# Kernel tuning notes

Measured on AMD Instinct MI355X. Metric: run time of the kernel, lower is better.

## Reference

```python
import jax, jax.numpy as jnp
import numpy as np
from jax import lax

B, L, D = 2, 512, 1024
N, K, R = 16, 4, 64
DEPTH, V, MLP = 4, 50000, 4096
HALF = D // 2


def _ln(x, s, b, eps=1e-5):
    m = x.mean(-1, keepdims=True)
    v = ((x - m) ** 2).mean(-1, keepdims=True)
    return (x - m) / jnp.sqrt(v + eps) * s + b


def _selective_scan(x, wx, wz, wp, cw, dtw, dtb, a_log, dpar, wout):
    bsz, seqlen, d = x.shape
    x_res = x @ wx.T
    z = x @ wz.T
    p = x @ wp.T  # [B,L,R+2N]
    dt_u, b_proj, c_proj = p[..., :R], p[..., R:R + N], p[..., R + N:]
    dt = jax.nn.softplus(dt_u @ dtw.T + dtb)  # [B,L,D]
    # causal depthwise conv (torch pads K-1 both sides then slices :L == left-pad K-1)
    conv = lax.conv_general_dilated(x_res.transpose(0, 2, 1), cw[:, None, :],
                                    (1,), [(K - 1, 0)], feature_group_count=d)
    u = jax.nn.silu(conv.transpose(0, 2, 1))  # [B,L,D]
    a = -jnp.exp(a_log)  # [D,N]
    a_t = jnp.exp(dt[..., None] * a)  # [B,L,D,N] (ZOH discretize)
    b_t = jnp.where(jnp.abs(a) < 1e-8, dt[..., None], (a_t - 1.0) / (a + 1e-10))
    inp = b_t * b_proj[:, :, None, :] * u[..., None]  # [B,L,D,N]

    def step(h, xs):
        at, it, ct = xs
        h = at * h + it
        return h, jnp.einsum('bn,bdn->bd', ct, h)

    h0 = jnp.zeros((bsz, d, N), a_t.dtype)
    _, ys = lax.scan(step, h0, (a_t.transpose(1, 0, 2, 3),
                                inp.transpose(1, 0, 2, 3),
                                c_proj.transpose(1, 0, 2)))
    y = ys.transpose(1, 0, 2)  # [B,L,D]
    y = (y + u * dpar) * jax.nn.silu(z)
    return y @ wout.T


def _forward(input_ids, timesteps, emb_table, tw1, tb1, tw2, tb2,
             ln1_s, ln1_b, wx, wz, wp, conv_w, dt_w, dt_b, A_log, Dp, wout,
             ln2_s, ln2_b, mlp_w1, mlp_b1, mlp_w2, mlp_b2,
             lnout_s, lnout_b, head_w, head_b):
    # sinusoidal time embedding [B,D]
    freq = jnp.exp(jnp.arange(HALF, dtype=jnp.float32) * (-np.log(10000.0) / (HALF - 1)))
    e = timesteps.astype(jnp.float32)[:, None] * freq
    temb = jnp.concatenate([jnp.sin(e), jnp.cos(e)], axis=-1)
    temb = jax.nn.silu(temb @ tw1.T + tb1) @ tw2.T + tb2
    x = emb_table[input_ids] + temb[:, None, :]
    for i in range(DEPTH):
        h = _selective_scan(_ln(x, ln1_s[i], ln1_b[i]), wx[i], wz[i], wp[i],
                            conv_w[i], dt_w[i], dt_b[i], A_log[i], Dp[i], wout[i])
        x = x + h
        m = _ln(x, ln2_s[i], ln2_b[i])
        m = jax.nn.gelu(m @ mlp_w1[i].T + mlp_b1[i], approximate=False) @ mlp_w2[i].T + mlp_b2[i]
        x = x + m
    x = _ln(x, lnout_s, lnout_b)
    return x @ head_w.T + head_b  # [B,L,V]


def setup_inputs() -> dict:
    key = jax.random.key(0)
    ks = jax.random.split(key, 20)

    def nrm(k, shape, scale=0.02):
        return jax.random.normal(k, shape, jnp.float32) * scale

    dt_std = R ** (-0.5)
    inp = {
        'input_ids': jax.random.randint(ks[0], (B, L), 0, V + 1),
        'timesteps': jax.random.randint(ks[1], (B,), 0, 100),
        'emb_table': nrm(ks[2], (V + 1, D)),
        'tw1': nrm(ks[3], (4 * D, D)), 'tb1': jnp.zeros((4 * D,), jnp.float32),
        'tw2': nrm(ks[4], (D, 4 * D)), 'tb2': jnp.zeros((D,), jnp.float32),
        'ln1_s': jnp.ones((DEPTH, D), jnp.float32), 'ln1_b': jnp.zeros((DEPTH, D), jnp.float32),
        'wx': nrm(ks[5], (DEPTH, D, D)),
        'wz': nrm(ks[6], (DEPTH, D, D)),
        'wp': nrm(ks[7], (DEPTH, R + 2 * N, D)),
        'conv_w': nrm(ks[8], (DEPTH, D, K), 0.1),
        'dt_w': jax.random.uniform(ks[9], (DEPTH, D, R), jnp.float32, -dt_std, dt_std),
        'dt_b': jnp.full((DEPTH, D), float(np.log(np.expm1(0.01))), jnp.float32),
        'A_log': jnp.tile(jnp.log(jnp.arange(1, N + 1, dtype=jnp.float32))[None, None, :], (DEPTH, D, 1)),
        'Dp': jnp.ones((DEPTH, D), jnp.float32),
        'wout': nrm(ks[10], (DEPTH, D, D)),
        'ln2_s': jnp.ones((DEPTH, D), jnp.float32), 'ln2_b': jnp.zeros((DEPTH, D), jnp.float32),
        'mlp_w1': nrm(ks[11], (DEPTH, MLP, D)), 'mlp_b1': jnp.zeros((DEPTH, MLP), jnp.float32),
        'mlp_w2': nrm(ks[12], (DEPTH, D, MLP)), 'mlp_b2': jnp.zeros((DEPTH, D), jnp.float32),
        'lnout_s': jnp.ones((D,), jnp.float32), 'lnout_b': jnp.zeros((D,), jnp.float32),
        'head_w': nrm(ks[13], (V, D)), 'head_b': jnp.zeros((V,), jnp.float32),
    }
    return inp


def reference(input_ids, timesteps, emb_table, tw1, tb1, tw2, tb2,
              ln1_s, ln1_b, wx, wz, wp, conv_w, dt_w, dt_b, A_log, Dp, wout,
              ln2_s, ln2_b, mlp_w1, mlp_b1, mlp_w2, mlp_b2,
              lnout_s, lnout_b, head_w, head_b):
    return _forward(input_ids, timesteps, emb_table, tw1, tb1, tw2, tb2,
                    ln1_s, ln1_b, wx, wz, wp, conv_w, dt_w, dt_b, A_log, Dp, wout,
                    ln2_s, ln2_b, mlp_w1, mlp_b1, mlp_w2, mlp_b2,
                    lnout_s, lnout_b, head_w, head_b)
```

## Files before the change

kernel.cpp:

```cpp
#include <hip/hip_runtime.h>

typedef unsigned short u16;
typedef __attribute__((ext_vector_type(8))) __bf16 bf16x8;
typedef __attribute__((ext_vector_type(4))) float floatx4;

#define B_ 2
#define L_ 512
#define D_ 1024
#define N_ 16
#define R_ 64
#define DEPTH_ 4
#define V_ 50000
#define MLP_ 4096
#define MROWS (B_ * L_)
#define SCAN_C 32
#define SCAN_S (L_ / SCAN_C)

#define SWZ(b) ((b) ^ ((((b) >> 7) & 7) << 4))

__device__ __forceinline__ float b2f(u16 u) {
    unsigned int i = ((unsigned int)u) << 16;
    return __builtin_bit_cast(float, i);
}
__device__ __forceinline__ u16 f2b(float f) {
    return __builtin_bit_cast(u16, (__bf16)f);
}
__device__ __forceinline__ uint2 f4_to_b4(float4 v) {
    u16 a = f2b(v.x), b = f2b(v.y), c = f2b(v.z), d = f2b(v.w);
    uint2 r;
    r.x = (unsigned int)a | ((unsigned int)b << 16);
    r.y = (unsigned int)c | ((unsigned int)d << 16);
    return r;
}
__device__ __forceinline__ void async16(const void* g, void* l) {
    __builtin_amdgcn_global_load_lds(
        (const __attribute__((address_space(1))) void*)g,
        (__attribute__((address_space(3))) void*)l, 16, 0, 0);
}
template <int Ncnt>
__device__ __forceinline__ void waitcnt_vm() {
    if constexpr (Ncnt == 0) asm volatile("s_waitcnt vmcnt(0)" ::: "memory");
    else if constexpr (Ncnt == 2) asm volatile("s_waitcnt vmcnt(2)" ::: "memory");
    else if constexpr (Ncnt == 3) asm volatile("s_waitcnt vmcnt(3)" ::: "memory");
    else if constexpr (Ncnt == 4) asm volatile("s_waitcnt vmcnt(4)" ::: "memory");
    else if constexpr (Ncnt == 6) asm volatile("s_waitcnt vmcnt(6)" ::: "memory");
    else if constexpr (Ncnt == 8) asm volatile("s_waitcnt vmcnt(8)" ::: "memory");
    else asm volatile("s_waitcnt vmcnt(0)" ::: "memory");
}
__device__ __forceinline__ float silu_f(float v) { return v / (1.f + expf(-v)); }
__device__ __forceinline__ float gelu_f(float v) {
    return 0.5f * v * (1.f + erff(v * 0.7071067811865476f));
}
__device__ __forceinline__ float softplus_f(float v) {
    return fmaxf(v, 0.f) + log1pf(expf(-fabsf(v)));
}

__global__ __launch_bounds__(256) void cvt_kernel(const float* __restrict__ in,
                                                  u16* __restrict__ out, const int n8) {
    const int i = blockIdx.x * 256 + threadIdx.x;
    if (i >= n8) return;
    const float4 a = *reinterpret_cast<const float4*>(&in[(size_t)i * 8]);
    const float4 b = *reinterpret_cast<const float4*>(&in[(size_t)i * 8 + 4]);
    uint4 o;
    uint2 lo = f4_to_b4(a), hi = f4_to_b4(b);
    o.x = lo.x; o.y = lo.y; o.z = hi.x; o.w = hi.y;
    *reinterpret_cast<uint4*>(&out[(size_t)i * 8]) = o;
}

template <int BM, int BN, int ACT, int RES, int PIPEOK, typename AT, typename WT, typename OUT>
__global__ __launch_bounds__(256) void gemm_bt(
    const AT* __restrict__ A, const int lda,
    const WT* __restrict__ W, const WT* __restrict__ W2,
    const float* __restrict__ bias,
    OUT* __restrict__ out, OUT* __restrict__ out2,
    const int N, const int K, const int nt, const int gsz) {
    constexpr int BK = 64;
    constexpr int MI = BM / 32;
    constexpr int NI = BN / 32;
    constexpr int WM = BM / 2;
    constexpr bool PIPE = PIPEOK && (sizeof(AT) == 2) && (sizeof(WT) == 2);
    __shared__ alignas(16) u16 lA[(PIPE ? 2 : 1) * BM * BK];
    __shared__ alignas(16) u16 lW[(PIPE ? 2 : 1) * BN * BK];
    const int tid = threadIdx.x;
    const int lane = tid & 63, wv = tid >> 6;
    const int bid = blockIdx.x;

    int mI, nI;
    if (gsz > 0) {
        const int mtt = gridDim.x / nt;
        const int fullG = nt / gsz;
        const int fullBlocks = fullG * gsz * mtt;
        if (bid < fullBlocks) {
            const int per = gsz * mtt;
            const int g = bid / per, r = bid % per;
            mI = r / gsz;
            nI = g * gsz + r % gsz;
        } else {
            const int rem = nt - fullG * gsz;
            const int r = bid - fullBlocks;
            mI = r / rem;
            nI = fullG * gsz + r % rem;
        }
    } else {
        mI = bid / nt;
        nI = bid % nt;
    }
    const int m0 = mI * BM;
    int n0 = nI * BN;
    const WT* Wp = W;
    OUT* op = out;
    if (W2 != nullptr && n0 >= N) {
        Wp = W2;
        op = out2;
        n0 -= N;
    }
    const int wr = wv >> 1, wc = wv & 1;
    const int lr = lane & 15, kg = lane >> 4;

    floatx4 acc[MI][NI];
#pragma unroll
    for (int i = 0; i < MI; ++i)
#pragma unroll
        for (int j = 0; j < NI; ++j) {
            floatx4 z4 = {0.f, 0.f, 0.f, 0.f};
            acc[i][j] = z4;
        }

    const int T = K / BK;

    if constexpr (PIPE) {
        constexpr int NEWER = BM / 32 + BN / 32;
        auto issue = [&](int t) {
            const int buf = t & 1;
            const int kt = t * BK;
#pragma unroll
            for (int c = wv; c < BM / 8; c += 4) {
                const int dst = c * 1024 + lane * 16;
                const int lg = SWZ(dst);
                const int row = lg >> 7, colb = lg & 127;
                async16((const char*)A + ((size_t)(m0 + row) * lda + kt) * 2 + colb,
                        (char*)lA + buf * BM * 128 + c * 1024);
            }
#pragma unroll
            for (int c = wv; c < BN / 8; c += 4) {
                const int dst = c * 1024 + lane * 16;
                const int lg = SWZ(dst);
                const int row = lg >> 7, colb = lg & 127;
                int rn = n0 + row;
                rn = (rn < N) ? rn : (N - 1);
                async16((const char*)Wp + ((size_t)rn * K + kt) * 2 + colb,
                        (char*)lW + buf * BN * 128 + c * 1024);
            }
        };
        issue(0);
        for (int t = 0; t < T; ++t) {
            if (t + 1 < T) {
                issue(t + 1);
                waitcnt_vm<NEWER>();
            } else {
                waitcnt_vm<0>();
            }
            __builtin_amdgcn_s_barrier();
            __builtin_amdgcn_sched_barrier(0);
            const char* bA = (const char*)lA + (t & 1) * BM * 128;
            const char* bW = (const char*)lW + (t & 1) * BN * 128;
#pragma unroll
            for (int kk = 0; kk < 2; ++kk) {
                bf16x8 aF[MI], bF[NI];
#pragma unroll
                for (int mi = 0; mi < MI; ++mi)
                    aF[mi] = *reinterpret_cast<const bf16x8*>(
                        bA + SWZ((wr * WM + mi * 16 + lr) * 128 + kk * 64 + kg * 16));
#pragma unroll
                for (int ni = 0; ni < NI; ++ni)
                    bF[ni] = *reinterpret_cast<const bf16x8*>(
                        bW + SWZ((wc * (BN / 2) + ni * 16 + lr) * 128 + kk * 64 + kg * 16));
#pragma unroll
                for (int mi = 0; mi < MI; ++mi)
#pragma unroll
                    for (int ni = 0; ni < NI; ++ni)
                        acc[mi][ni] = __builtin_amdgcn_mfma_f32_16x16x32_bf16(
                            aF[mi], bF[ni], acc[mi][ni], 0, 0, 0);
            }
            __builtin_amdgcn_sched_barrier(0);
            if (t + 1 < T) __builtin_amdgcn_s_barrier();
        }
    } else {
        for (int t = 0; t < T; ++t) {
            const int kt = t * BK;
            if (t) __syncthreads();
            if constexpr (sizeof(AT) == 2) {
#pragma unroll
                for (int c = wv; c < BM / 8; c += 4) {
                    const int dst = c * 1024 + lane * 16;
                    const int lg = SWZ(dst);
                    const int row = lg >> 7, colb = lg & 127;
                    async16((const char*)A + ((size_t)(m0 + row) * lda + kt) * 2 + colb,
                            (char*)lA + c * 1024);
                }
            } else {
                constexpr int ACHF = (BM * BK) / 1024;
                float4 raF[ACHF];
#pragma unroll
                for (int i = 0; i < ACHF; ++i) {
                    const int idx = tid + i * 256;
                    const int row = idx >> 4, c4 = (idx & 15) * 4;
                    raF[i] = *reinterpret_cast<const float4*>(&A[(size_t)(m0 + row) * lda + kt + c4]);
                }
#pragma unroll
                for (int i = 0; i < ACHF; ++i) {
                    const int idx = tid + i * 256;
                    const int row = idx >> 4, c4 = (idx & 15) * 4;
                    *reinterpret_cast<uint2*>((char*)lA + SWZ(row * 128 + c4 * 2)) = f4_to_b4(raF[i]);
                }
            }
            if constexpr (sizeof(WT) == 2) {
#pragma unroll
                for (int c = wv; c < BN / 8; c += 4) {
                    const int dst = c * 1024 + lane * 16;
                    const int lg = SWZ(dst);
                    const int row = lg >> 7, colb = lg & 127;
                    int rn = n0 + row;
                    rn = (rn < N) ? rn : (N - 1);
                    async16((const char*)Wp + ((size_t)rn * K + kt) * 2 + colb,
                            (char*)lW + c * 1024);
                }
            } else {
                constexpr int WCHF = (BN * BK) / 1024;
                float4 rwF[WCHF];
#pragma unroll
                for (int i = 0; i < WCHF; ++i) {
                    const int idx = tid + i * 256;
                    const int row = idx >> 4, c4 = (idx & 15) * 4;
                    int rn = n0 + row;
                    rn = (rn < N) ? rn : (N - 1);
                    rwF[i] = *reinterpret_cast<const float4*>(&Wp[(size_t)rn * K + kt + c4]);
                }
#pragma unroll
                for (int i = 0; i < WCHF; ++i) {
                    const int idx = tid + i * 256;
                    const int row = idx >> 4, c4 = (idx & 15) * 4;
                    *reinterpret_cast<uint2*>((char*)lW + SWZ(row * 128 + c4 * 2)) = f4_to_b4(rwF[i]);
                }
            }
            __syncthreads();
#pragma unroll
            for (int kk = 0; kk < 2; ++kk) {
                bf16x8 aF[MI], bF[NI];
#pragma unroll
                for (int mi = 0; mi < MI; ++mi)
                    aF[mi] = *reinterpret_cast<const bf16x8*>(
                        (const char*)lA + SWZ((wr * WM + mi * 16 + lr) * 128 + kk * 64 + kg * 16));
#pragma unroll
                for (int ni = 0; ni < NI; ++ni)
                    bF[ni] = *reinterpret_cast<const bf16x8*>(
                        (const char*)lW + SWZ((wc * (BN / 2) + ni * 16 + lr) * 128 + kk * 64 + kg * 16));
#pragma unroll
                for (int mi = 0; mi < MI; ++mi)
#pragma unroll
                    for (int ni = 0; ni < NI; ++ni)
                        acc[mi][ni] = __builtin_amdgcn_mfma_f32_16x16x32_bf16(
                            aF[mi], bF[ni], acc[mi][ni], 0, 0, 0);
            }
        }
    }

#pragma unroll
    for (int mi = 0; mi < MI; ++mi) {
        const int rb = m0 + wr * WM + mi * 16 + kg * 4;
#pragma unroll
        for (int r = 0; r < 4; ++r) {
            const size_t rowoff = (size_t)(rb + r) * (size_t)N;
#pragma unroll
            for (int ni = 0; ni < NI; ++ni) {
                const int col = n0 + wc * (BN / 2) + ni * 16 + lr;
                if (col >= N) continue;
                float v = acc[mi][ni][r] + (bias ? bias[col] : 0.f);
                if constexpr (ACT == 1) v = gelu_f(v);
                if constexpr (ACT == 2) v = softplus_f(v);
                const size_t o = rowoff + (size_t)col;
                if constexpr (RES) {
                    op[o] += v;
                } else if constexpr (sizeof(OUT) == 2) {
                    op[o] = f2b(v);
                } else {
                    op[o] = v;
                }
            }
        }
    }
}

__global__ __launch_bounds__(256) void temb0_kernel(const int* __restrict__ ts,
                                                    float* __restrict__ temb0) {
    int i = blockIdx.x * 256 + threadIdx.x;
    if (i >= B_ * D_) return;
    int b = i >> 10, k = i & 1023;
    float t = (float)ts[b];
    int h = (k < 512) ? k : (k - 512);
    float f = expf((float)h * (-9.210340371976184f / 511.f));
    float e = t * f;
    temb0[i] = (k < 512) ? sinf(e) : cosf(e);
}

template <int ACTV>
__global__ __launch_bounds__(256) void rowdot_kernel(const float* __restrict__ in,
                                                     const float* __restrict__ W,
                                                     const float* __restrict__ bias,
                                                     float* __restrict__ out,
                                                     const int Ncols, const int K) {
    const int g = (blockIdx.x * 256 + threadIdx.x) >> 6;
    const int lane = threadIdx.x & 63;
    if (g >= B_ * Ncols) return;
    const int b = g / Ncols, j = g % Ncols;
    const float* xr = in + (size_t)b * K;
    const float* wr = W + (size_t)j * K;
    float s = 0.f;
    for (int k = lane; k < K; k += 64) s += xr[k] * wr[k];
#pragma unroll
    for (int o = 32; o; o >>= 1) s += __shfl_xor(s, o);
    if (lane == 0) {
        float v = s + bias[j];
        if (ACTV == 1) v = silu_f(v);
        out[(size_t)b * Ncols + j] = v;
    }
}

__global__ __launch_bounds__(256) void embed_kernel(const int* __restrict__ ids,
                                                    const float* __restrict__ emb,
                                                    const float* __restrict__ temb2,
                                                    float* __restrict__ x) {
    const int gid = blockIdx.x * 256 + threadIdx.x;
    const int d8 = gid & 127;
    const int row = gid >> 7;
    const int b = row >> 9;
    const int d0 = d8 * 8;
    const int id = ids[row];
    const float4 e0 = *reinterpret_cast<const float4*>(&emb[(size_t)id * D_ + d0]);
    const float4 e1 = *reinterpret_cast<const float4*>(&emb[(size_t)id * D_ + d0 + 4]);
    const float4 t0 = *reinterpret_cast<const float4*>(&temb2[b * D_ + d0]);
    const float4 t1 = *reinterpret_cast<const float4*>(&temb2[b * D_ + d0 + 4]);
    float4 o0, o1;
    o0.x = e0.x + t0.x; o0.y = e0.y + t0.y; o0.z = e0.z + t0.z; o0.w = e0.w + t0.w;
    o1.x = e1.x + t1.x; o1.y = e1.y + t1.y; o1.z = e1.z + t1.z; o1.w = e1.w + t1.w;
    *reinterpret_cast<float4*>(&x[(size_t)row * D_ + d0]) = o0;
    *reinterpret_cast<float4*>(&x[(size_t)row * D_ + d0 + 4]) = o1;
}

__global__ __launch_bounds__(256) void ln_kernel(const float* __restrict__ x,
                                                 const float* __restrict__ s,
                                                 const float* __restrict__ bb,
                                                 u16* __restrict__ out) {
    __shared__ float red[4];
    const int row = blockIdx.x, tid = threadIdx.x;
    const float4 v = *reinterpret_cast<const float4*>(x + (size_t)row * D_ + tid * 4);
    float sm = v.x + v.y + v.z + v.w;
#pragma unroll
    for (int o = 1; o < 64; o <<= 1) sm += __shfl_xor(sm, o);
    if ((tid & 63) == 0) red[tid >> 6] = sm;
    __syncthreads();
    const float mean = (red[0] + red[1] + red[2] + red[3]) * (1.f / 1024.f);
    __syncthreads();
    const float dx = v.x - mean, dy = v.y - mean, dz = v.z - mean, dw = v.w - mean;
    float sq = dx * dx + dy * dy + dz * dz + dw * dw;
#pragma unroll
    for (int o = 1; o < 64; o <<= 1) sq += __shfl_xor(sq, o);
    if ((tid & 63) == 0) red[tid >> 6] = sq;
    __syncthreads();
    const float var = (red[0] + red[1] + red[2] + red[3]) * (1.f / 1024.f);
    const float rs = rsqrtf(var + 1e-5f);
    const int c = tid * 4;
    const float4 sv = *reinterpret_cast<const float4*>(&s[c]);
    const float4 bv = *reinterpret_cast<const float4*>(&bb[c]);
    float4 o;
    o.x = dx * rs * sv.x + bv.x;
    o.y = dy * rs * sv.y + bv.y;
    o.z = dz * rs * sv.z + bv.z;
    o.w = dw * rs * sv.w + bv.w;
    *reinterpret_cast<uint2*>(&out[(size_t)row * D_ + c]) = f4_to_b4(o);
}

__global__ __launch_bounds__(256) void scan_p1(const u16* __restrict__ dt,
                                               const float* __restrict__ p,
                                               const u16* __restrict__ xr,
                                               const float* __restrict__ cw,
                                               const float* __restrict__ alog,
                                               float* __restrict__ Aprod,
                                               float* __restrict__ Hloc) {
    const int tid = threadIdx.x;
    const int ng = tid & 3;
    const int dl = tid >> 2;
    int blk = blockIdx.x;
    const int chunk = blk % SCAN_C; blk /= SCAN_C;
    const int dg = blk % (D_ / 64);
    const int b = blk / (D_ / 64);
    const int d = dg * 64 + dl;

    float a_v[4], inv_a[4];
#pragma unroll
    for (int j = 0; j < 4; ++j) {
        float av = -expf(alog[d * N_ + ng * 4 + j]);
        a_v[j] = av;
        inv_a[j] = 1.f / (av + 1e-10f);
    }
    const float4 cw4 = *reinterpret_cast<const float4*>(&cw[d * 4]);

    __shared__ float pbuf[SCAN_S * 32];
    const int t0 = chunk * SCAN_S;
    if (tid < SCAN_S * 8) {
        const int s = tid >> 3, off = (tid & 7) * 4;
        *reinterpret_cast<float4*>(&pbuf[s * 32 + off]) =
            *reinterpret_cast<const float4*>(&p[((size_t)(b * L_ + t0 + s)) * 96 + 64 + off]);
    }
    __syncthreads();

    const size_t base = (size_t)b * L_ * D_ + d;
    float xm3 = (t0 >= 3) ? b2f(xr[base + (size_t)(t0 - 3) * D_]) : 0.f;
    float xm2 = (t0 >= 2) ? b2f(xr[base + (size_t)(t0 - 2) * D_]) : 0.f;
    float xm1 = (t0 >= 1) ? b2f(xr[base + (size_t)(t0 - 1) * D_]) : 0.f;

    float A[4] = {1.f, 1.f, 1.f, 1.f};
    float h[4] = {0.f, 0.f, 0.f, 0.f};
#pragma unroll
    for (int s = 0; s < SCAN_S; ++s) {
        const size_t idx = base + (size_t)(t0 + s) * D_;
        const float xc = b2f(xr[idx]);
        const float uv = silu_f(cw4.x * xm3 + cw4.y * xm2 + cw4.z * xm1 + cw4.w * xc);
        xm3 = xm2; xm2 = xm1; xm1 = xc;
        const float dtv = b2f(dt[idx]);
#pragma unroll
        for (int j = 0; j < 4; ++j) {
            const float ex = fminf(dtv * a_v[j], 0.f);
            const float at = expf(ex);
            const float bt = (fabsf(a_v[j]) < 1e-8f) ? dtv : (at - 1.f) * inv_a[j];
            const float bp = pbuf[s * 32 + ng * 4 + j];
            A[j] *= at;
            h[j] = at * h[j] + bt * bp * uv;
        }
    }
    const size_t o = ((size_t)(b * SCAN_C + chunk) * D_ + d) * N_ + ng * 4;
    float4 a4 = {A[0], A[1], A[2], A[3]};
    float4 h4 = {h[0], h[1], h[2], h[3]};
    *reinterpret_cast<float4*>(&Aprod[o]) = a4;
    *reinterpret_cast<float4*>(&Hloc[o]) = h4;
}

__global__ __launch_bounds__(256) void scan_p2(const float* __restrict__ Aprod,
                                               const float* __restrict__ Hloc,
                                               float* __restrict__ Hstart) {
    const int gid = blockIdx.x * 256 + threadIdx.x;
    if (gid >= B_ * D_ * N_) return;
    const int b = gid / (D_ * N_);
    const int rem = gid % (D_ * N_);
    float H = 0.f;
#pragma unroll 8
    for (int k = 0; k < SCAN_C; ++k) {
        const size_t o = (size_t)(b * SCAN_C + k) * (D_ * N_) + rem;
        Hstart[o] = H;
        H = Aprod[o] * H + Hloc[o];
    }
}

__global__ __launch_bounds__(256) void scan_p3(const u16* __restrict__ dt,
                                               const float* __restrict__ p,
                                               const u16* __restrict__ xr,
                                               const float* __restrict__ cw,
                                               const u16* __restrict__ z,
                                               const float* __restrict__ alog,
                                               const float* __restrict__ Dp,
                                               const float* __restrict__ Hstart,
                                               u16* __restrict__ yg) {
    const int tid = threadIdx.x;
    const int ng = tid & 3;
    const int dl = tid >> 2;
    int blk = blockIdx.x;
    const int chunk = blk % SCAN_C; blk /= SCAN_C;
    const int dg = blk % (D_ / 64);
    const int b = blk / (D_ / 64);
    const int d = dg * 64 + dl;

    float a_v[4], inv_a[4];
#pragma unroll
    for (int j = 0; j < 4; ++j) {
        float av = -expf(alog[d * N_ + ng * 4 + j]);
        a_v[j] = av;
        inv_a[j] = 1.f / (av + 1e-10f);
    }
    const float Dpd = Dp[d];
    const float4 cw4 = *reinterpret_cast<const float4*>(&cw[d * 4]);

    __shared__ float pbuf[SCAN_S * 32];
    const int t0 = chunk * SCAN_S;
    if (tid < SCAN_S * 8) {
        const int s = tid >> 3, off = (tid & 7) * 4;
        *reinterpret_cast<float4*>(&pbuf[s * 32 + off]) =
            *reinterpret_cast<const float4*>(&p[((size_t)(b * L_ + t0 + s)) * 96 + 64 + off]);
    }
    __syncthreads();

    const size_t base = (size_t)b * L_ * D_ + d;
    float xm3 = (t0 >= 3) ? b2f(xr[base + (size_t)(t0 - 3) * D_]) : 0.f;
    float xm2 = (t0 >= 2) ? b2f(xr[base + (size_t)(t0 - 2) * D_]) : 0.f;
    float xm1 = (t0 >= 1) ? b2f(xr[base + (size_t)(t0 - 1) * D_]) : 0.f;

    float h[4];
    {
        const size_t o = ((size_t)(b * SCAN_C + chunk) * D_ + d) * N_ + ng * 4;
        const float4 h4 = *reinterpret_cast<const float4*>(&Hstart[o]);
        h[0] = h4.x; h[1] = h4.y; h[2] = h4.z; h[3] = h4.w;
    }

#pragma unroll
    for (int s = 0; s < SCAN_S; ++s) {
        const size_t idx = base + (size_t)(t0 + s) * D_;
        const float xc = b2f(xr[idx]);
        const float uv = silu_f(cw4.x * xm3 + cw4.y * xm2 + cw4.z * xm1 + cw4.w * xc);
        xm3 = xm2; xm2 = xm1; xm1 = xc;
        const float dtv = b2f(dt[idx]);
        float yp = 0.f;
#pragma unroll
        for (int j = 0; j < 4; ++j) {
            const float ex = fminf(dtv * a_v[j], 0.f);
            const float at = expf(ex);
            const float bt = (fabsf(a_v[j]) < 1e-8f) ? dtv : (at - 1.f) * inv_a[j];
            const float bp = pbuf[s * 32 + ng * 4 + j];
            const float cp = pbuf[s * 32 + 16 + ng * 4 + j];
            h[j] = at * h[j] + bt * bp * uv;
            yp += cp * h[j];
        }
        yp += __shfl_xor(yp, 1);
        yp += __shfl_xor(yp, 2);
        if (ng == 0) {
            const float zv = b2f(z[idx]);
            yg[idx] = f2b((yp + uv * Dpd) * silu_f(zv));
        }
    }
}

extern "C" void kernel_launch(void* const* d_in, const int* in_sizes, int n_in,
                              void* d_out, int out_size, void* d_ws, size_t ws_size,
                              hipStream_t stream) {
    (void)in_sizes; (void)n_in; (void)out_size;
    const int* ids = (const int*)d_in[0];
    const int* tsteps = (const int*)d_in[1];
    const float* emb = (const float*)d_in[2];
    const float* tw1 = (const float*)d_in[3];
    const float* tb1 = (const float*)d_in[4];
    const float* tw2 = (const float*)d_in[5];
    const float* tb2 = (const float*)d_in[6];
    const float* ln1s = (const float*)d_in[7];
    const float* ln1b = (const float*)d_in[8];
    const float* wx = (const float*)d_in[9];
    const float* wz = (const float*)d_in[10];
    const float* wp = (const float*)d_in[11];
    const float* convw = (const float*)d_in[12];
    const float* dtw = (const float*)d_in[13];
    const float* dtb = (const float*)d_in[14];
    const float* alog = (const float*)d_in[15];
    const float* dp = (const float*)d_in[16];
    const float* wo = (const float*)d_in[17];
    const float* ln2s = (const float*)d_in[18];
    const float* ln2b = (const float*)d_in[19];
    const float* mw1 = (const float*)d_in[20];
    const float* mb1 = (const float*)d_in[21];
    const float* mw2 = (const float*)d_in[22];
    const float* mb2 = (const float*)d_in[23];
    const float* lnos = (const float*)d_in[24];
    const float* lnob = (const float*)d_in[25];
    const float* hw = (const float*)d_in[26];
    const float* hb = (const float*)d_in[27];
    float* outp = (float*)d_out;

    char* w = (char*)d_ws;
    size_t used = 0;
    auto alloc = [&](size_t bytes) {
        char* pp = w;
        size_t rb = (bytes + 255) & ~(size_t)255;
        w += rb;
        used += rb;
        return pp;
    };
    float* x = (float*)alloc((size_t)MROWS * D_ * 4);
    float* t0f = (float*)alloc((size_t)B_ * D_ * 4);
    float* t1f = (float*)alloc((size_t)B_ * MLP_ * 4);
    float* t2f = (float*)alloc((size_t)B_ * D_ * 4);
    u16* xnb = (u16*)alloc((size_t)MROWS * D_ * 2);
    u16* xres = (u16*)alloc((size_t)MROWS * D_ * 2);
    u16* zb = (u16*)alloc((size_t)MROWS * D_ * 2);
    float* pf = (float*)alloc((size_t)MROWS * 96 * 4);
    u16* dtb16 = (u16*)alloc((size_t)MROWS * D_ * 2);
    u16* ygb = (u16*)alloc((size_t)MROWS * D_ * 2);
    const bool cvt_head = (ws_size >= used + (size_t)V_ * D_ * 2 + 4096);
    u16* hwb = cvt_head ? (u16*)alloc((size_t)V_ * D_ * 2) : nullptr;
    const size_t lw_bytes = ((size_t)DEPTH_ * D_ * D_ * 3 + (size_t)DEPTH_ * 96 * D_ +
                             (size_t)DEPTH_ * D_ * R_ + (size_t)DEPTH_ * MLP_ * D_ * 2) * 2;
    const bool cvt_layer = cvt_head && (ws_size >= used + lw_bytes + ((size_t)1 << 20));
    u16 *wxb = nullptr, *wzb = nullptr, *wpb = nullptr, *dtwb = nullptr, *wob = nullptr,
        *mw1b = nullptr, *mw2b = nullptr;
    if (cvt_layer) {
        wxb = (u16*)alloc((size_t)DEPTH_ * D_ * D_ * 2);
        wzb = (u16*)alloc((size_t)DEPTH_ * D_ * D_ * 2);
        wpb = (u16*)alloc((size_t)DEPTH_ * 96 * D_ * 2);
        dtwb = (u16*)alloc((size_t)DEPTH_ * D_ * R_ * 2);
        wob = (u16*)alloc((size_t)DEPTH_ * D_ * D_ * 2);
        mw1b = (u16*)alloc((size_t)DEPTH_ * MLP_ * D_ * 2);
        mw2b = (u16*)alloc((size_t)DEPTH_ * MLP_ * D_ * 2);
    }
    u16* m1b = (u16*)outp;
    float* Aprod = outp + (size_t)6 * 1024 * 1024;
    float* Hloc = outp + (size_t)8 * 1024 * 1024;
    float* Hstart = outp + (size_t)10 * 1024 * 1024;

    auto cvt = [&](const float* src, u16* dst, size_t n) {
        cvt_kernel<<<dim3((unsigned)((n / 8 + 255) / 256)), dim3(256), 0, stream>>>(src, dst,
                                                                                   (int)(n / 8));
    };
    if (cvt_head) cvt(hw, hwb, (size_t)V_ * D_);
    if (cvt_layer) {
        cvt(wx, wxb, (size_t)DEPTH_ * D_ * D_);
        cvt(wz, wzb, (size_t)DEPTH_ * D_ * D_);
        cvt(wp, wpb, (size_t)DEPTH_ * 96 * D_);
        cvt(dtw, dtwb, (size_t)DEPTH_ * D_ * R_);
        cvt(wo, wob, (size_t)DEPTH_ * D_ * D_);
        cvt(mw1, mw1b, (size_t)DEPTH_ * MLP_ * D_);
        cvt(mw2, mw2b, (size_t)DEPTH_ * MLP_ * D_);
    }
    temb0_kernel<<<dim3((B_ * D_ + 255) / 256), dim3(256), 0, stream>>>(tsteps, t0f);
    rowdot_kernel<1><<<dim3(B_ * MLP_ / 4), dim3(256), 0, stream>>>(t0f, tw1, tb1, t1f, MLP_, D_);
    rowdot_kernel<0><<<dim3(B_ * D_ / 4), dim3(256), 0, stream>>>(t1f, tw2, tb2, t2f, D_, MLP_);
    embed_kernel<<<dim3(MROWS * D_ / 8 / 256), dim3(256), 0, stream>>>(ids, emb, t2f, x);

    for (int i = 0; i < DEPTH_; ++i) {
        const float* cwi = convw + (size_t)i * D_ * 4;
        const float* dtbi = dtb + (size_t)i * D_;
        const float* ali = alog + (size_t)i * D_ * N_;
        const float* dpi = dp + (size_t)i * D_;
        const float* mb1i = mb1 + (size_t)i * MLP_;
        const float* mb2i = mb2 + (size_t)i * D_;

        ln_kernel<<<dim3(MROWS), dim3(256), 0, stream>>>(x, ln1s + i * D_, ln1b + i * D_, xnb);
        if (cvt_layer) {
            gemm_bt<32, 64, 0, 0, 1, u16, u16, u16><<<dim3(1024), dim3(256), 0, stream>>>(
                xnb, D_, wxb + (size_t)i * D_ * D_, wzb + (size_t)i * D_ * D_, nullptr,
                xres, zb, D_, D_, 32, 0);
            gemm_bt<32, 64, 0, 0, 1, u16, u16, float><<<dim3(64), dim3(256), 0, stream>>>(
                xnb, D_, wpb + (size_t)i * 96 * D_, nullptr, nullptr, pf, nullptr, 96, D_, 2, 0);
            gemm_bt<32, 64, 2, 0, 1, float, u16, u16><<<dim3(512), dim3(256), 0, stream>>>(
                pf, 96, dtwb + (size_t)i * D_ * R_, nullptr, dtbi, dtb16, nullptr, D_, R_, 16, 0);
        } else {
            gemm_bt<32, 64, 0, 0, 1, u16, float, u16><<<dim3(1024), dim3(256), 0, stream>>>(
                xnb, D_, wx + (size_t)i * D_ * D_, wz + (size_t)i * D_ * D_, nullptr,
                xres, zb, D_, D_, 32, 0);
            gemm_bt<32, 64, 0, 0, 1, u16, float, float><<<dim3(64), dim3(256), 0, stream>>>(
                xnb, D_, wp + (size_t)i * 96 * D_, nullptr, nullptr, pf, nullptr, 96, D_, 2, 0);
            gemm_bt<32, 64, 2, 0, 1, float, float, u16><<<dim3(512), dim3(256), 0, stream>>>(
                pf, 96, dtw + (size_t)i * D_ * R_, nullptr, dtbi, dtb16, nullptr, D_, R_, 16, 0);
        }
        scan_p1<<<dim3(B_ * (D_ / 64) * SCAN_C), dim3(256), 0, stream>>>(
            dtb16, pf, xres, cwi, ali, Aprod, Hloc);
        scan_p2<<<dim3(B_ * D_ * N_ / 256), dim3(256), 0, stream>>>(Aprod, Hloc, Hstart);
        scan_p3<<<dim3(B_ * (D_ / 64) * SCAN_C), dim3(256), 0, stream>>>(
            dtb16, pf, xres, cwi, zb, ali, dpi, Hstart, ygb);
        if (cvt_layer) {
            gemm_bt<32, 64, 0, 1, 1, u16, u16, float><<<dim3(512), dim3(256), 0, stream>>>(
                ygb, D_, wob + (size_t)i * D_ * D_, nullptr, nullptr, x, nullptr, D_, D_, 16, 0);
        } else {
            gemm_bt<32, 64, 0, 1, 1, u16, float, float><<<dim3(512), dim3(256), 0, stream>>>(
                ygb, D_, wo + (size_t)i * D_ * D_, nullptr, nullptr, x, nullptr, D_, D_, 16, 0);
        }
        ln_kernel<<<dim3(MROWS), dim3(256), 0, stream>>>(x, ln2s + i * D_, ln2b + i * D_, xnb);
        if (cvt_layer) {
            gemm_bt<32, 64, 1, 0, 1, u16, u16, u16><<<dim3(2048), dim3(256), 0, stream>>>(
                xnb, D_, mw1b + (size_t)i * MLP_ * D_, nullptr, mb1i, m1b, nullptr, MLP_, D_, 64, 0);
            gemm_bt<32, 64, 0, 1, 1, u16, u16, float><<<dim3(512), dim3(256), 0, stream>>>(
                m1b, MLP_, mw2b + (size_t)i * MLP_ * D_, nullptr, mb2i, x, nullptr, D_, MLP_, 16, 0);
        } else {
            gemm_bt<32, 64, 1, 0, 1, u16, float, u16><<<dim3(2048), dim3(256), 0, stream>>>(
                xnb, D_, mw1 + (size_t)i * MLP_ * D_, nullptr, mb1i, m1b, nullptr, MLP_, D_, 64, 0);
            gemm_bt<32, 64, 0, 1, 1, u16, float, float><<<dim3(512), dim3(256), 0, stream>>>(
                m1b, MLP_, mw2 + (size_t)i * MLP_ * D_, nullptr, mb2i, x, nullptr, D_, MLP_, 16, 0);
        }
    }

    ln_kernel<<<dim3(MROWS), dim3(256), 0, stream>>>(x, lnos, lnob, xnb);
    constexpr int HNT = (V_ + 127) / 128;
    if (cvt_head) {
        gemm_bt<128, 128, 0, 0, 1, u16, u16, float>
            <<<dim3(8 * HNT), dim3(256), 0, stream>>>(
                xnb, D_, hwb, (const u16*)nullptr, hb, outp, nullptr, V_, D_, HNT, 32);
    } else {
        gemm_bt<128, 128, 0, 0, 0, u16, float, float>
            <<<dim3(8 * HNT), dim3(256), 0, stream>>>(
                xnb, D_, hw, (const float*)nullptr, hb, outp, nullptr, V_, D_, HNT, 32);
    }
}
```

Measured before the change: 974.7 us.

## Use triple-buffered async LDS pipeline for layer GEMMs, drop grouped tile raster

Deepens the async global-to-LDS prefetch in the bf16 GEMM from two to three buffers, issuing two tiles ahead with matching vmcnt waits. The intent is to hide more global-load latency. Removes the grouped block-to-tile remapping and switches the vocab head GEMM to the non-pipelined path. The extra buffer raises LDS use and may lower occupancy, and the head GEMM loses both its L2-friendly raster and its prefetch pipeline.

```diff
diff --git a/kernel.cpp b/kernel.cpp
--- a/kernel.cpp
+++ b/kernel.cpp
@@ -45,6 +45,8 @@
     else if constexpr (Ncnt == 4) asm volatile("s_waitcnt vmcnt(4)" ::: "memory");
     else if constexpr (Ncnt == 6) asm volatile("s_waitcnt vmcnt(6)" ::: "memory");
     else if constexpr (Ncnt == 8) asm volatile("s_waitcnt vmcnt(8)" ::: "memory");
+    else if constexpr (Ncnt == 12) asm volatile("s_waitcnt vmcnt(12)" ::: "memory");
+    else if constexpr (Ncnt == 16) asm volatile("s_waitcnt vmcnt(16)" ::: "memory");
     else asm volatile("s_waitcnt vmcnt(0)" ::: "memory");
 }
 __device__ __forceinline__ float silu_f(float v) { return v / (1.f + expf(-v)); }
@@ -67,46 +69,27 @@
     *reinterpret_cast<uint4*>(&out[(size_t)i * 8]) = o;
 }
 
-template <int BM, int BN, int ACT, int RES, int PIPEOK, typename AT, typename WT, typename OUT>
+template <int BM, int BN, int ACT, int RES, int PD, typename AT, typename WT, typename OUT>
 __global__ __launch_bounds__(256) void gemm_bt(
     const AT* __restrict__ A, const int lda,
     const WT* __restrict__ W, const WT* __restrict__ W2,
     const float* __restrict__ bias,
     OUT* __restrict__ out, OUT* __restrict__ out2,
-    const int N, const int K, const int nt, const int gsz) {
+    const int N, const int K, const int nt) {
     constexpr int BK = 64;
     constexpr int MI = BM / 32;
     constexpr int NI = BN / 32;
     constexpr int WM = BM / 2;
-    constexpr bool PIPE = PIPEOK && (sizeof(AT) == 2) && (sizeof(WT) == 2);
-    __shared__ alignas(16) u16 lA[(PIPE ? 2 : 1) * BM * BK];
-    __shared__ alignas(16) u16 lW[(PIPE ? 2 : 1) * BN * BK];
+    constexpr bool PIPE = (PD == 2) && (sizeof(AT) == 2) && (sizeof(WT) == 2);
+    constexpr int NBUF = PIPE ? 3 : 1;
+    __shared__ alignas(16) u16 lA[NBUF * BM * BK];
+    __shared__ alignas(16) u16 lW[NBUF * BN * BK];
     const int tid = threadIdx.x;
     const int lane = tid & 63, wv = tid >> 6;
     const int bid = blockIdx.x;
 
-    int mI, nI;
-    if (gsz > 0) {
-        const int mtt = gridDim.x / nt;
-        const int fullG = nt / gsz;
-        const int fullBlocks = fullG * gsz * mtt;
-        if (bid < fullBlocks) {
-            const int per = gsz * mtt;
-            const int g = bid / per, r = bid % per;
-            mI = r / gsz;
-            nI = g * gsz + r % gsz;
-        } else {
-            const int rem = nt - fullG * gsz;
-            const int r = bid - fullBlocks;
-            mI = r / rem;
-            nI = fullG * gsz + r % rem;
-        }
-    } else {
-        mI = bid / nt;
-        nI = bid % nt;
-    }
-    const int m0 = mI * BM;
-    int n0 = nI * BN;
+    const int m0 = (bid / nt) * BM;
+    int n0 = (bid % nt) * BN;
     const WT* Wp = W;
     OUT* op = out;
     if (W2 != nullptr && n0 >= N) {
@@ -129,9 +112,9 @@
     const int T = K / BK;
 
     if constexpr (PIPE) {
-        constexpr int NEWER = BM / 32 + BN / 32;
+        constexpr int P = BM / 32 + BN / 32;
         auto issue = [&](int t) {
-            const int buf = t & 1;
+            const int buf = t % 3;
             const int kt = t * BK;
 #pragma unroll
             for (int c = wv; c < BM / 8; c += 4) {
@@ -153,17 +136,20 @@
             }
         };
         issue(0);
+        if (T > 1) issue(1);
         for (int t = 0; t < T; ++t) {
-            if (t + 1 < T) {
-                issue(t + 1);
-                waitcnt_vm<NEWER>();
+            if (t + 2 < T) {
+                issue(t + 2);
+                waitcnt_vm<2 * P>();
+            } else if (t + 1 < T) {
+                waitcnt_vm<P>();
             } else {
                 waitcnt_vm<0>();
             }
             __builtin_amdgcn_s_barrier();
             __builtin_amdgcn_sched_barrier(0);
-            const char* bA = (const char*)lA + (t & 1) * BM * 128;
-            const char* bW = (const char*)lW + (t & 1) * BN * 128;
+            const char* bA = (const char*)lA + (t % 3) * BM * 128;
+            const char* bW = (const char*)lW + (t % 3) * BN * 128;
 #pragma unroll
             for (int kk = 0; kk < 2; ++kk) {
                 bf16x8 aF[MI], bF[NI];
@@ -640,21 +626,21 @@
 
         ln_kernel<<<dim3(MROWS), dim3(256), 0, stream>>>(x, ln1s + i * D_, ln1b + i * D_, xnb);
         if (cvt_layer) {
-            gemm_bt<32, 64, 0, 0, 1, u16, u16, u16><<<dim3(1024), dim3(256), 0, stream>>>(
+            gemm_bt<32, 64, 0, 0, 2, u16, u16, u16><<<dim3(1024), dim3(256), 0, stream>>>(
                 xnb, D_, wxb + (size_t)i * D_ * D_, wzb + (size_t)i * D_ * D_, nullptr,
-                xres, zb, D_, D_, 32, 0);
-            gemm_bt<32, 64, 0, 0, 1, u16, u16, float><<<dim3(64), dim3(256), 0, stream>>>(
-                xnb, D_, wpb + (size_t)i * 96 * D_, nullptr, nullptr, pf, nullptr, 96, D_, 2, 0);
-            gemm_bt<32, 64, 2, 0, 1, float, u16, u16><<<dim3(512), dim3(256), 0, stream>>>(
-                pf, 96, dtwb + (size_t)i * D_ * R_, nullptr, dtbi, dtb16, nullptr, D_, R_, 16, 0);
+                xres, zb, D_, D_, 32);
+            gemm_bt<32, 64, 0, 0, 2, u16, u16, float><<<dim3(64), dim3(256), 0, stream>>>(
+                xnb, D_, wpb + (size_t)i * 96 * D_, nullptr, nullptr, pf, nullptr, 96, D_, 2);
+            gemm_bt<32, 64, 2, 0, 0, float, u16, u16><<<dim3(512), dim3(256), 0, stream>>>(
+                pf, 96, dtwb + (size_t)i * D_ * R_, nullptr, dtbi, dtb16, nullptr, D_, R_, 16);
         } else {
-            gemm_bt<32, 64, 0, 0, 1, u16, float, u16><<<dim3(1024), dim3(256), 0, stream>>>(
+            gemm_bt<32, 64, 0, 0, 0, u16, float, u16><<<dim3(1024), dim3(256), 0, stream>>>(
                 xnb, D_, wx + (size_t)i * D_ * D_, wz + (size_t)i * D_ * D_, nullptr,
-                xres, zb, D_, D_, 32, 0);
-            gemm_bt<32, 64, 0, 0, 1, u16, float, float><<<dim3(64), dim3(256), 0, stream>>>(
-                xnb, D_, wp + (size_t)i * 96 * D_, nullptr, nullptr, pf, nullptr, 96, D_, 2, 0);
-            gemm_bt<32, 64, 2, 0, 1, float, float, u16><<<dim3(512), dim3(256), 0, stream>>>(
-                pf, 96, dtw + (size_t)i * D_ * R_, nullptr, dtbi, dtb16, nullptr, D_, R_, 16, 0);
+                xres, zb, D_, D_, 32);
+            gemm_bt<32, 64, 0, 0, 0, u16, float, float><<<dim3(64), dim3(256), 0, stream>>>(
+                xnb, D_, wp + (size_t)i * 96 * D_, nullptr, nullptr, pf, nullptr, 96, D_, 2);
+            gemm_bt<32, 64, 2, 0, 0, float, float, u16><<<dim3(512), dim3(256), 0, stream>>>(
+                pf, 96, dtw + (size_t)i * D_ * R_, nullptr, dtbi, dtb16, nullptr, D_, R_, 16);
         }
         scan_p1<<<dim3(B_ * (D_ / 64) * SCAN_C), dim3(256), 0, stream>>>(
             dtb16, pf, xres, cwi, ali, Aprod, Hloc);
@@ -662,35 +648,35 @@
         scan_p3<<<dim3(B_ * (D_ / 64) * SCAN_C), dim3(256), 0, stream>>>(
             dtb16, pf, xres, cwi, zb, ali, dpi, Hstart, ygb);
         if (cvt_layer) {
-            gemm_bt<32, 64, 0, 1, 1, u16, u16, float><<<dim3(512), dim3(256), 0, stream>>>(
-                ygb, D_, wob + (size_t)i * D_ * D_, nullptr, nullptr, x, nullptr, D_, D_, 16, 0);
+            gemm_bt<32, 64, 0, 1, 2, u16, u16, float><<<dim3(512), dim3(256), 0, stream>>>(
+                ygb, D_, wob + (size_t)i * D_ * D_, nullptr, nullptr, x, nullptr, D_, D_, 16);
         } else {
-            gemm_bt<32, 64, 0, 1, 1, u16, float, float><<<dim3(512), dim3(256), 0, stream>>>(
-                ygb, D_, wo + (size_t)i * D_ * D_, nullptr, nullptr, x, nullptr, D_, D_, 16, 0);
+            gemm_bt<32, 64, 0, 1, 0, u16, float, float><<<dim3(512), dim3(256), 0, stream>>>(
+                ygb, D_, wo + (size_t)i * D_ * D_, nullptr, nullptr, x, nullptr, D_, D_, 16);
         }
         ln_kernel<<<dim3(MROWS), dim3(256), 0, stream>>>(x, ln2s + i * D_, ln2b + i * D_, xnb);
         if (cvt_layer) {
-            gemm_bt<32, 64, 1, 0, 1, u16, u16, u16><<<dim3(2048), dim3(256), 0, stream>>>(
-                xnb, D_, mw1b + (size_t)i * MLP_ * D_, nullptr, mb1i, m1b, nullptr, MLP_, D_, 64, 0);
-            gemm_bt<32, 64, 0, 1, 1, u16, u16, float><<<dim3(512), dim3(256), 0, stream>>>(
-                m1b, MLP_, mw2b + (size_t)i * MLP_ * D_, nullptr, mb2i, x, nullptr, D_, MLP_, 16, 0);
+            gemm_bt<32, 64, 1, 0, 2, u16, u16, u16><<<dim3(2048), dim3(256), 0, stream>>>(
+                xnb, D_, mw1b + (size_t)i * MLP_ * D_, nullptr, mb1i, m1b, nullptr, MLP_, D_, 64);
+            gemm_bt<32, 64, 0, 1, 2, u16, u16, float><<<dim3(512), dim3(256), 0, stream>>>(
+                m1b, MLP_, mw2b + (size_t)i * MLP_ * D_, nullptr, mb2i, x, nullptr, D_, MLP_, 16);
         } else {
-            gemm_bt<32, 64, 1, 0, 1, u16, float, u16><<<dim3(2048), dim3(256), 0, stream>>>(
-                xnb, D_, mw1 + (size_t)i * MLP_ * D_, nullptr, mb1i, m1b, nullptr, MLP_, D_, 64, 0);
-            gemm_bt<32, 64, 0, 1, 1, u16, float, float><<<dim3(512), dim3(256), 0, stream>>>(
-                m1b, MLP_, mw2 + (size_t)i * MLP_ * D_, nullptr, mb2i, x, nullptr, D_, MLP_, 16, 0);
+            gemm_bt<32, 64, 1, 0, 0, u16, float, u16><<<dim3(2048), dim3(256), 0, stream>>>(
+                xnb, D_, mw1 + (size_t)i * MLP_ * D_, nullptr, mb1i, m1b, nullptr, MLP_, D_, 64);
+            gemm_bt<32, 64, 0, 1, 0, u16, float, float><<<dim3(512), dim3(256), 0, stream>>>(
+                m1b, MLP_, mw2 + (size_t)i * MLP_ * D_, nullptr, mb2i, x, nullptr, D_, MLP_, 16);
         }
     }
 
     ln_kernel<<<dim3(MROWS), dim3(256), 0, stream>>>(x, lnos, lnob, xnb);
     constexpr int HNT = (V_ + 127) / 128;
     if (cvt_head) {
-        gemm_bt<128, 128, 0, 0, 1, u16, u16, float>
+        gemm_bt<128, 128, 0, 0, 0, u16, u16, float>
             <<<dim3(8 * HNT), dim3(256), 0, stream>>>(
-                xnb, D_, hwb, (const u16*)nullptr, hb, outp, nullptr, V_, D_, HNT, 32);
+                xnb, D_, hwb, (const u16*)nullptr, hb, outp, nullptr, V_, D_, HNT);
     } else {
         gemm_bt<128, 128, 0, 0, 0, u16, float, float>
             <<<dim3(8 * HNT), dim3(256), 0, stream>>>(
-                xnb, D_, hw, (const float*)nullptr, hb, outp, nullptr, V_, D_, HNT, 32);
-    }
-}
+                xnb, D_, hw, (const float*)nullptr, hb, outp, nullptr, V_, D_, HNT);
+    }
+}
```

Result: slower. 1.067 ms (+9.4%).
